# Performance work log

Hardware: AMD Instinct MI355X
Metric: run time of the kernel (lower is better)

Reference implementation:

```python
import jax, jax.numpy as jnp
import numpy as np

K1, K2 = 2, 4  # kernels of the two channel groups
BN_EPS = 1e-5


def _neocell_group(x, wa, wb, k):
    # Block-diagonal (a @ x) @ b with a k x k block repeated along the diagonal
    # per channel (NeoCellRepeat): equivalent to blockwise transforms on H and W.
    B, c, H, W = x.shape
    xb = x.reshape(B, c, H // k, k, W // k, k)
    y = jnp.einsum('cpi,bcnimj,cjq->bcnpmq', wa, xb, wb)
    return y.reshape(B, c, H, W)


def setup_inputs() -> dict:
    key = jax.random.key(0)
    ks = jax.random.split(key, 12)
    B, C, H, W = 32, 256, 56, 56
    c1, c2 = 128, 128
    Ci = 4 * C  # inner_mult = 4
    x = jax.random.normal(ks[0], (B, C, H, W), dtype=jnp.float32)
    wa1 = jax.random.normal(ks[1], (c1, K1, K1), dtype=jnp.float32) / np.float32(np.sqrt(K1))
    wb1 = jax.random.normal(ks[2], (c1, K1, K1), dtype=jnp.float32) / np.float32(np.sqrt(K1))
    wa2 = jax.random.normal(ks[3], (c2, K2, K2), dtype=jnp.float32) / np.float32(np.sqrt(K2))
    wb2 = jax.random.normal(ks[4], (c2, K2, K2), dtype=jnp.float32) / np.float32(np.sqrt(K2))
    bn_weight = 1.0 + 0.1 * jax.random.normal(ks[5], (C,), dtype=jnp.float32)
    bn_bias = 0.1 * jax.random.normal(ks[6], (C,), dtype=jnp.float32)
    bn_mean = 0.1 * jax.random.normal(ks[7], (C,), dtype=jnp.float32)
    bn_var = jax.random.uniform(ks[8], (C,), dtype=jnp.float32, minval=0.5, maxval=1.5)
    fc1_w = jax.random.normal(ks[9], (Ci, C), dtype=jnp.float32) / np.float32(np.sqrt(C))
    fc2_w = jax.random.normal(ks[10], (C, Ci), dtype=jnp.float32) / np.float32(np.sqrt(Ci))
    return {"x": x, "wa1": wa1, "wb1": wb1, "wa2": wa2, "wb2": wb2,
            "bn_weight": bn_weight, "bn_bias": bn_bias, "bn_mean": bn_mean,
            "bn_var": bn_var, "fc1_w": fc1_w, "fc2_w": fc2_w}


def reference(x, wa1, wb1, wa2, wb2, bn_weight, bn_bias, bn_mean, bn_var, fc1_w, fc2_w):
    c1 = wa1.shape[0]
    # NeoCell: per-group block-diagonal (a @ x) @ b
    y = jnp.concatenate([
        _neocell_group(x[:, :c1], wa1, wb1, K1),
        _neocell_group(x[:, c1:], wa2, wb2, K2),
    ], axis=1)
    # BatchNorm2d (eval mode, running stats)
    inv = jax.lax.rsqrt(bn_var + BN_EPS)
    scale = (bn_weight * inv)[None, :, None, None]
    shift = (bn_bias - bn_mean * bn_weight * inv)[None, :, None, None]
    y = y * scale + shift
    # chw -> hwc, MLP with exact GELU, hwc -> chw
    y = jnp.transpose(y, (0, 2, 3, 1))
    h = jax.nn.gelu(y @ fc1_w.T, approximate=False)
    y = h @ fc2_w.T
    y = jnp.transpose(y, (0, 3, 1, 2))
    # residual (drop_path = 0)
    return y + x
```

## Files before the change

### kernel.cpp

```cpp
#include <hip/hip_runtime.h>
#include <stdint.h>

typedef __bf16 bf16x8 __attribute__((ext_vector_type(8)));
typedef float f32x4 __attribute__((ext_vector_type(4)));

__device__ __forceinline__ float bf2f(uint16_t u) {
  union { uint32_t i; float f; } v; v.i = ((uint32_t)u) << 16; return v.f;
}
__device__ __forceinline__ uint16_t f2bf(float f) {
  union { float f; uint32_t i; } v; v.f = f;
  uint32_t u = v.i;
  uint32_t r = (u + 0x7FFFu + ((u >> 16) & 1u)) >> 16;
  return (uint16_t)r;
}
__device__ __forceinline__ float fast_gelu(float v) {
  float t2 = v * v;
  float pz = 1.0f + 0.044715f * t2;
  float w = -1.5957691216f * v * pz;
  float e = __expf(w);
  return v * __builtin_amdgcn_rcpf(1.0f + e);
}

__global__ __launch_bounds__(256) void cvt_weights_kernel(
    const float* __restrict__ fc1, const float* __restrict__ fc2,
    uint16_t* __restrict__ fc1b, uint16_t* __restrict__ fc2b)
{
  int i = (blockIdx.x * 256 + threadIdx.x) * 4;
  if (i < 262144) {
    float4 a = *(const float4*)(fc1 + i);
    ushort4 o;
    o.x = f2bf(a.x); o.y = f2bf(a.y); o.z = f2bf(a.z); o.w = f2bf(a.w);
    *(ushort4*)(fc1b + i) = o;
  } else {
    int j = i - 262144;
    float4 a = *(const float4*)(fc2 + j);
    ushort4 o;
    o.x = f2bf(a.x); o.y = f2bf(a.y); o.z = f2bf(a.z); o.w = f2bf(a.w);
    *(ushort4*)(fc2b + j) = o;
  }
}

__global__ __launch_bounds__(128) void neocell_bn_kernel(
    const float* __restrict__ x,
    const float* __restrict__ wa1, const float* __restrict__ wb1,
    const float* __restrict__ wa2, const float* __restrict__ wb2,
    const float* __restrict__ bnw, const float* __restrict__ bnb,
    const float* __restrict__ bnm, const float* __restrict__ bnv,
    uint16_t* __restrict__ y1)
{
  __shared__ uint16_t lx[64 * 226];
  const int t = threadIdx.x;
  const int strip = blockIdx.x;
  const int b = blockIdx.y;
  const int grp = blockIdx.z;
  const int h0 = strip * 4;

  for (int i = 0; i < 28; ++i) {
    int l = t + i * 128;
    int c = l / 56;
    int r = l - c * 56;
    const float* g = x + (size_t)(b * 256 + grp * 64 + c) * 3136
                       + h0 * 56 + r * 4;
    float4 v = *(const float4*)g;
    ushort4 o;
    o.x = f2bf(v.x); o.y = f2bf(v.y); o.z = f2bf(v.z); o.w = f2bf(v.w);
    *(ushort4*)(lx + c * 226 + r * 4) = o;
  }
  __syncthreads();

  const int c = t & 63;
  const int p = t >> 6;
  const int cg = grp * 64 + c;

  const float sc = bnw[cg] * rsqrtf(bnv[cg] + 1e-5f);
  const float sh = bnb[cg] - bnm[cg] * sc;
  const size_t pgbase = (size_t)b * 3136 + (size_t)h0 * 56;
  const uint16_t* lc0 = lx + c * 226;

  if (grp < 2) {
    float A[2][2], Bm[2][2];
#pragma unroll
    for (int i = 0; i < 2; ++i)
#pragma unroll
      for (int j = 0; j < 2; ++j) {
        A[i][j]  = wa1[cg * 4 + i * 2 + j];
        Bm[i][j] = wb1[cg * 4 + i * 2 + j];
      }
    for (int m = 0; m < 28; ++m) {
      const uint16_t* lc = lc0 + (2 * p) * 56 + m * 2;
      uint32_t w0 = *(const uint32_t*)lc;
      uint32_t w1 = *(const uint32_t*)(lc + 56);
      float X[2][2];
      X[0][0] = bf2f((uint16_t)w0); X[0][1] = bf2f((uint16_t)(w0 >> 16));
      X[1][0] = bf2f((uint16_t)w1); X[1][1] = bf2f((uint16_t)(w1 >> 16));
      float T[2][2];
#pragma unroll
      for (int pp = 0; pp < 2; ++pp)
#pragma unroll
        for (int j = 0; j < 2; ++j)
          T[pp][j] = A[pp][0] * X[0][j] + A[pp][1] * X[1][j];
#pragma unroll
      for (int pp = 0; pp < 2; ++pp)
#pragma unroll
        for (int q = 0; q < 2; ++q) {
          float O = (T[pp][0] * Bm[0][q] + T[pp][1] * Bm[1][q]) * sc + sh;
          size_t pg = pgbase + (size_t)(2 * p + pp) * 56 + (m * 2 + q);
          y1[pg * 256 + cg] = f2bf(O);
        }
    }
  } else {
    const int ck = cg - 128;
    float A[4][4], Bm[4][4];
#pragma unroll
    for (int i = 0; i < 4; ++i)
#pragma unroll
      for (int j = 0; j < 4; ++j) {
        A[i][j]  = wa2[ck * 16 + i * 4 + j];
        Bm[i][j] = wb2[ck * 16 + i * 4 + j];
      }
    for (int mm = 0; mm < 7; ++mm) {
      int m = 2 * mm + p;
      float X[4][4];
#pragma unroll
      for (int i = 0; i < 4; ++i) {
        const uint16_t* lc = lc0 + i * 56 + m * 4;
        uint32_t w0 = *(const uint32_t*)lc;
        uint32_t w1 = *(const uint32_t*)(lc + 2);
        X[i][0] = bf2f((uint16_t)w0); X[i][1] = bf2f((uint16_t)(w0 >> 16));
        X[i][2] = bf2f((uint16_t)w1); X[i][3] = bf2f((uint16_t)(w1 >> 16));
      }
      float T[4][4];
#pragma unroll
      for (int pp = 0; pp < 4; ++pp)
#pragma unroll
        for (int j = 0; j < 4; ++j)
          T[pp][j] = A[pp][0] * X[0][j] + A[pp][1] * X[1][j]
                   + A[pp][2] * X[2][j] + A[pp][3] * X[3][j];
#pragma unroll
      for (int pp = 0; pp < 4; ++pp)
#pragma unroll
        for (int q = 0; q < 4; ++q) {
          float O = (T[pp][0] * Bm[0][q] + T[pp][1] * Bm[1][q]
                   + T[pp][2] * Bm[2][q] + T[pp][3] * Bm[3][q]) * sc + sh;
          size_t pg = pgbase + (size_t)pp * 56 + (m * 4 + q);
          y1[pg * 256 + cg] = f2bf(O);
        }
    }
  }
}

template <int KD, int EPI>
__global__ __launch_bounds__(256) void gemm_bt_kernel(
    const uint16_t* __restrict__ A,
    const uint16_t* __restrict__ Bw,
    uint16_t* __restrict__ Cb16,
    float* __restrict__ Cf32,
    const float* __restrict__ Xres,
    int chunk_pix0)
{
  __shared__ uint16_t lds[16640];
  uint16_t* ldsA = lds;
  uint16_t* ldsB = lds + 4096;

  const int tid = threadIdx.x;
  const int lane = tid & 63;
  const int wid = tid >> 6;
  const int wm = wid & 1;
  const int wn = wid >> 1;
  const int fm = lane & 15;
  const int fq = lane >> 4;

  uint32_t nx = gridDim.x;
  uint32_t n = nx * gridDim.y;
  uint32_t lid = blockIdx.y * nx + blockIdx.x;
  uint32_t bx, by;
  if ((n & 7u) == 0u) {
    uint32_t w = (lid & 7u) * (n >> 3) + (lid >> 3);
    bx = w & (nx - 1u);
    by = w / nx;
  } else {
    bx = blockIdx.x; by = blockIdx.y;
  }

  const size_t arow0 = (size_t)by * 128;
  const size_t brow0 = (size_t)bx * 128;

  f32x4 acc[4][4];
#pragma unroll
  for (int i = 0; i < 4; ++i)
#pragma unroll
    for (int j = 0; j < 4; ++j) { f32x4 z = {0.f, 0.f, 0.f, 0.f}; acc[i][j] = z; }

  const int q0 = tid, q1 = tid + 256;
  const int r0 = q0 >> 2, kk0 = q0 & 3;
  const int r1 = q1 >> 2, kk1 = q1 & 3;
  const uint16_t* a0 = A + (arow0 + r0) * KD + kk0 * 8;
  const uint16_t* a1 = A + (arow0 + r1) * KD + kk1 * 8;
  const uint16_t* b0 = Bw + (brow0 + r0) * KD + kk0 * 8;
  const uint16_t* b1 = Bw + (brow0 + r1) * KD + kk1 * 8;

  for (int k0 = 0; k0 < KD; k0 += 32) {
    __syncthreads();
    __builtin_amdgcn_global_load_lds(
        (const __attribute__((address_space(1))) void*)(a0 + k0),
        (__attribute__((address_space(3))) void*)(ldsA + q0 * 8), 16, 0, 0);
    __builtin_amdgcn_global_load_lds(
        (const __attribute__((address_space(1))) void*)(a1 + k0),
        (__attribute__((address_space(3))) void*)(ldsA + q1 * 8), 16, 0, 0);
    __builtin_amdgcn_global_load_lds(
        (const __attribute__((address_space(1))) void*)(b0 + k0),
        (__attribute__((address_space(3))) void*)(ldsB + q0 * 8), 16, 0, 0);
    __builtin_amdgcn_global_load_lds(
        (const __attribute__((address_space(1))) void*)(b1 + k0),
        (__attribute__((address_space(3))) void*)(ldsB + q1 * 8), 16, 0, 0);
    __syncthreads();

    bf16x8 af[4], bfr[4];
#pragma unroll
    for (int mt = 0; mt < 4; ++mt)
      af[mt] = *(const bf16x8*)(const void*)
               (ldsA + (wm * 64 + mt * 16 + fm) * 32 + fq * 8);
#pragma unroll
    for (int nt = 0; nt < 4; ++nt)
      bfr[nt] = *(const bf16x8*)(const void*)
                (ldsB + (wn * 64 + nt * 16 + fm) * 32 + fq * 8);
#pragma unroll
    for (int mt = 0; mt < 4; ++mt)
#pragma unroll
      for (int nt = 0; nt < 4; ++nt)
        acc[mt][nt] = __builtin_amdgcn_mfma_f32_16x16x32_bf16(
            af[mt], bfr[nt], acc[mt][nt], 0, 0, 0);
  }

  if (EPI == 0) {
#pragma unroll
    for (int mt = 0; mt < 4; ++mt) {
      const size_t rb = arow0 + wm * 64 + mt * 16 + fq * 4;
#pragma unroll
      for (int nt = 0; nt < 4; ++nt) {
        const size_t n2 = brow0 + wn * 64 + nt * 16 + fm;
#pragma unroll
        for (int r = 0; r < 4; ++r)
          Cb16[(rb + r) * 1024 + n2] = f2bf(fast_gelu(acc[mt][nt][r]));
      }
    }
  } else {
    __syncthreads();
#pragma unroll
    for (int mt = 0; mt < 4; ++mt) {
      int mbase = wm * 64 + mt * 16 + fq * 4;
#pragma unroll
      for (int nt = 0; nt < 4; ++nt) {
        int nn = wn * 64 + nt * 16 + fm;
#pragma unroll
        for (int r = 0; r < 4; ++r)
          lds[nn * 130 + mbase + r] = f2bf(acc[mt][nt][r]);
      }
    }
    __syncthreads();
    const int pl0 = tid & 31;
    const int cw = tid >> 5;
#pragma unroll
    for (int it = 0; it < 16; ++it) {
      int ch = cw + it * 8;
      int cgl = (int)brow0 + ch;
#pragma unroll
      for (int e = 0; e < 4; ++e) {
        int pl = pl0 + e * 32;
        uint32_t pg = (uint32_t)chunk_pix0 + by * 128u + (uint32_t)pl;
        uint32_t bimg = pg / 3136u;
        uint32_t rem = pg - bimg * 3136u;
        size_t addr = ((size_t)bimg * 256 + cgl) * 3136 + rem;
        Cf32[addr] = bf2f(lds[ch * 130 + pl]) + Xres[addr];
      }
    }
  }
}

extern "C" void kernel_launch(void* const* d_in, const int* in_sizes, int n_in,
                              void* d_out, int out_size, void* d_ws,
                              size_t ws_size, hipStream_t stream)
{
  const float* x   = (const float*)d_in[0];
  const float* wa1 = (const float*)d_in[1];
  const float* wb1 = (const float*)d_in[2];
  const float* wa2 = (const float*)d_in[3];
  const float* wb2 = (const float*)d_in[4];
  const float* bnw = (const float*)d_in[5];
  const float* bnb = (const float*)d_in[6];
  const float* bnm = (const float*)d_in[7];
  const float* bnv = (const float*)d_in[8];
  const float* fc1 = (const float*)d_in[9];
  const float* fc2 = (const float*)d_in[10];
  float* out = (float*)d_out;

  uint16_t* fc1b = (uint16_t*)d_ws;
  uint16_t* fc2b = fc1b + 262144;
  uint16_t* y1 = fc2b + 262144;
  const size_t y1_elems = (size_t)100352 * 256;
  uint16_t* h = y1 + y1_elems;

  const long tiles_total = 784;
  const size_t fixed_bytes = (size_t)262144 * 4 + y1_elems * 2;
  long tiles_chunk = 1;
  if (ws_size > fixed_bytes + 262144) {
    tiles_chunk = (long)((ws_size - fixed_bytes) / (128ul * 1024ul * 2ul));
    if (tiles_chunk > 392) tiles_chunk = 392;
    if (tiles_chunk < 1) tiles_chunk = 1;
  }

  cvt_weights_kernel<<<512, 256, 0, stream>>>(fc1, fc2, fc1b, fc2b);
  neocell_bn_kernel<<<dim3(14, 32, 4), 128, 0, stream>>>(
      x, wa1, wb1, wa2, wb2, bnw, bnb, bnm, bnv, y1);

  for (long t0 = 0; t0 < tiles_total; t0 += tiles_chunk) {
    long T = tiles_total - t0;
    if (T > tiles_chunk) T = tiles_chunk;
    gemm_bt_kernel<256, 0><<<dim3(8, (uint32_t)T), 256, 0, stream>>>(
        y1 + (size_t)t0 * 128 * 256, fc1b, h, nullptr, nullptr, 0);
    gemm_bt_kernel<1024, 1><<<dim3(2, (uint32_t)T), 256, 0, stream>>>(
        h, fc2b, nullptr, out, x, (int)(t0 * 128));
  }
}
```

Before: 428.8 us.

## Double-buffer GEMM LDS tiles and allow a single full-size chunk

The GEMM main loop now uses two LDS buffers, so the next K-slice is loaded with global_load_lds while MFMAs run on the current slice, leaving one barrier per iteration instead of two. The last iterations issue redundant wrap-around loads so the loop stays branch-free. The tile-chunk cap is also raised from 392 to all 784 tiles, so a large enough workspace runs each GEMM as one launch. The risk is that the single barrier may not order the async LDS writes against other waves' reads unless the compiler inserts the needed vmcnt waits, and the wrap-around loads add some extra traffic.

```diff
diff --git a/kernel.cpp b/kernel.cpp
--- a/kernel.cpp
+++ b/kernel.cpp
@@ -19,6 +19,11 @@
   float w = -1.5957691216f * v * pz;
   float e = __expf(w);
   return v * __builtin_amdgcn_rcpf(1.0f + e);
+}
+__device__ __forceinline__ void gld16(uint16_t* l, const uint16_t* g) {
+  __builtin_amdgcn_global_load_lds(
+      (const __attribute__((address_space(1))) void*)g,
+      (__attribute__((address_space(3))) void*)l, 16, 0, 0);
 }
 
 __global__ __launch_bounds__(256) void cvt_weights_kernel(
@@ -159,8 +164,10 @@
     int chunk_pix0)
 {
   __shared__ uint16_t lds[16640];
-  uint16_t* ldsA = lds;
-  uint16_t* ldsB = lds + 4096;
+  uint16_t* A0 = lds;
+  uint16_t* B0 = lds + 4096;
+  uint16_t* A1 = lds + 8192;
+  uint16_t* B1 = lds + 12288;
 
   const int tid = threadIdx.x;
   const int lane = tid & 63;
@@ -199,37 +206,41 @@
   const uint16_t* b0 = Bw + (brow0 + r0) * KD + kk0 * 8;
   const uint16_t* b1 = Bw + (brow0 + r1) * KD + kk1 * 8;
 
-  for (int k0 = 0; k0 < KD; k0 += 32) {
-    __syncthreads();
-    __builtin_amdgcn_global_load_lds(
-        (const __attribute__((address_space(1))) void*)(a0 + k0),
-        (__attribute__((address_space(3))) void*)(ldsA + q0 * 8), 16, 0, 0);
-    __builtin_amdgcn_global_load_lds(
-        (const __attribute__((address_space(1))) void*)(a1 + k0),
-        (__attribute__((address_space(3))) void*)(ldsA + q1 * 8), 16, 0, 0);
-    __builtin_amdgcn_global_load_lds(
-        (const __attribute__((address_space(1))) void*)(b0 + k0),
-        (__attribute__((address_space(3))) void*)(ldsB + q0 * 8), 16, 0, 0);
-    __builtin_amdgcn_global_load_lds(
-        (const __attribute__((address_space(1))) void*)(b1 + k0),
-        (__attribute__((address_space(3))) void*)(ldsB + q1 * 8), 16, 0, 0);
-    __syncthreads();
-
+  auto phase = [&](const uint16_t* cA, const uint16_t* cB,
+                   uint16_t* nA, uint16_t* nB, int kn) {
+    gld16(nA + q0 * 8, a0 + kn);
+    gld16(nA + q1 * 8, a1 + kn);
+    gld16(nB + q0 * 8, b0 + kn);
+    gld16(nB + q1 * 8, b1 + kn);
     bf16x8 af[4], bfr[4];
 #pragma unroll
     for (int mt = 0; mt < 4; ++mt)
       af[mt] = *(const bf16x8*)(const void*)
-               (ldsA + (wm * 64 + mt * 16 + fm) * 32 + fq * 8);
+               (cA + (wm * 64 + mt * 16 + fm) * 32 + fq * 8);
 #pragma unroll
     for (int nt = 0; nt < 4; ++nt)
       bfr[nt] = *(const bf16x8*)(const void*)
-                (ldsB + (wn * 64 + nt * 16 + fm) * 32 + fq * 8);
+                (cB + (wn * 64 + nt * 16 + fm) * 32 + fq * 8);
 #pragma unroll
     for (int mt = 0; mt < 4; ++mt)
 #pragma unroll
       for (int nt = 0; nt < 4; ++nt)
         acc[mt][nt] = __builtin_amdgcn_mfma_f32_16x16x32_bf16(
             af[mt], bfr[nt], acc[mt][nt], 0, 0, 0);
+    __syncthreads();
+  };
+
+  gld16(A0 + q0 * 8, a0);
+  gld16(A0 + q1 * 8, a1);
+  gld16(B0 + q0 * 8, b0);
+  gld16(B0 + q1 * 8, b1);
+  __syncthreads();
+
+  constexpr int NT = KD / 32;
+#pragma unroll 1
+  for (int t = 0; t < NT; t += 2) {
+    phase(A0, B0, A1, B1, ((t + 1) & (NT - 1)) * 32);
+    phase(A1, B1, A0, B0, ((t + 2) & (NT - 1)) * 32);
   }
 
   if (EPI == 0) {
@@ -305,7 +316,7 @@
   long tiles_chunk = 1;
   if (ws_size > fixed_bytes + 262144) {
     tiles_chunk = (long)((ws_size - fixed_bytes) / (128ul * 1024ul * 2ul));
-    if (tiles_chunk > 392) tiles_chunk = 392;
+    if (tiles_chunk > tiles_total) tiles_chunk = tiles_total;
     if (tiles_chunk < 1) tiles_chunk = 1;
   }
 
```

After: 412.3 us. -3.9%, faster.
